# Kernel optimization log

Measured on AMD Instinct MI355X. Metric: run time of the kernel, lower is better.

## Reference

```python
import jax, jax.numpy as jnp
import numpy as np

B, N, C, H = 8, 1024, 768, 12
HD = C // H  # 64
SCALE = HD ** -0.5
T = 4
N_HALF = T // 2  # loop body with attention runs N_HALF times, V accumulates T times


def setup_inputs() -> dict:
    key = jax.random.key(0)
    ks = jax.random.split(key, 8)
    s = 0.02
    return {
        "x": jax.random.normal(ks[0], (B, N, C), jnp.float32),
        "Wqkv": jax.random.normal(ks[1], (3 * C, C), jnp.float32) * s,
        "Wfc1": jax.random.normal(ks[2], (HD, HD), jnp.float32) * s,
        "bfc1": jax.random.normal(ks[3], (HD,), jnp.float32) * s,
        "Wfc2": jax.random.normal(ks[4], (HD, HD), jnp.float32) * s,
        "bfc2": jax.random.normal(ks[5], (HD,), jnp.float32) * s,
        "Wproj": jax.random.normal(ks[6], (C, C), jnp.float32) * s,
        "bproj": jax.random.normal(ks[7], (C,), jnp.float32) * s,
    }


def reference(x, Wqkv, Wfc1, bfc1, Wfc2, bfc2, Wproj, bproj):
    b, n, c = x.shape
    # qkv projection (no bias), split into per-head q,k,v: [B,H,N,hd]
    qkv = (x @ Wqkv.T).reshape(b, n, 3, H, HD).transpose(2, 0, 3, 1, 4)
    q, k, v = qkv[0], qkv[1], qkv[2]
    # Loop body is stateless per timestep: first N_HALF steps each add the same
    # att_spk; all T steps add the same relu(v). Compute once, scale by counts.
    Q_spk = jax.nn.relu(q) @ Wfc1.T + bfc1  # [B,H,N,hd]
    K_spk = jax.nn.relu(k) @ Wfc2.T + bfc2  # [B,H,N,hd]
    att_spk = jax.nn.relu(jnp.einsum("bhqd,bhkd->bhqk", Q_spk, K_spk) * SCALE)
    att_rec = att_spk * float(N_HALF)   # accumulated over t < T/2
    V_rec = jax.nn.relu(v) * float(T)   # accumulated over all T steps
    att = jax.nn.softmax(att_rec, axis=-1)
    out = jnp.einsum("bhqk,bhkd->bhqd", att, V_rec)  # [B,H,N,hd]
    out = out.transpose(0, 2, 1, 3).reshape(b, n, c)
    return out @ Wproj.T + bproj
```

## Files before the change

### kernel.cpp

```cpp
#include <hip/hip_runtime.h>
#include <hip/hip_bf16.h>
#include <stdint.h>
#include <math.h>

#define BB   8
#define NN_  1024
#define CC   768
#define HH   12
#define HDD  64

typedef __attribute__((ext_vector_type(8))) short bf16x8;
typedef __attribute__((ext_vector_type(4))) float f32x4;
typedef __attribute__((ext_vector_type(16))) float f32x16;
typedef __attribute__((ext_vector_type(4))) float f32x4v;
typedef __attribute__((ext_vector_type(4))) unsigned short u16x4;

union FragU { unsigned int u[4]; bf16x8 b; };

__device__ __forceinline__ unsigned short f2bf(float f) {
    union { float f; unsigned int u; } v; v.f = f;
    unsigned int r = v.u + 0x7fffu + ((v.u >> 16) & 1u);
    return (unsigned short)(r >> 16);
}

#define CVTPK(d_, a_, b_) asm("v_cvt_pk_bf16_f32 %0, %1, %2" : "=v"(d_) : "v"(a_), "v"(b_))
#define SWAP32(a_, b_) asm("v_permlane32_swap_b32 %0, %1" : "+v"(a_), "+v"(b_))

#define GLDS(g_, l_) __builtin_amdgcn_global_load_lds( \
    (const __attribute__((address_space(1))) void*)(g_), \
    (__attribute__((address_space(3))) void*)(l_), 16, 0, 0)

#define MKFRAGS(P_, F0_, F1_) do {                                             \
    unsigned int c0,c1,c2,c3,c4,c5,c6,c7;                                      \
    CVTPK(c0, P_[0],  P_[1]);  CVTPK(c1, P_[2],  P_[3]);                       \
    CVTPK(c2, P_[4],  P_[5]);  CVTPK(c3, P_[6],  P_[7]);                       \
    CVTPK(c4, P_[8],  P_[9]);  CVTPK(c5, P_[10], P_[11]);                      \
    CVTPK(c6, P_[12], P_[13]); CVTPK(c7, P_[14], P_[15]);                      \
    SWAP32(c0, c2); SWAP32(c1, c3); SWAP32(c4, c6); SWAP32(c5, c7);            \
    FragU fu0_, fu1_;                                                          \
    fu0_.u[0]=c0; fu0_.u[1]=c1; fu0_.u[2]=c2; fu0_.u[3]=c3;                    \
    fu1_.u[0]=c4; fu1_.u[1]=c5; fu1_.u[2]=c6; fu1_.u[3]=c7;                    \
    F0_ = fu0_.b; F1_ = fu1_.b;                                                \
} while (0)

#define CVT_N0 1572864
#define CVT_N1 2015232
#define CVT_N2 2162688
#define CVT_N3 2163712
#define CVT_N4 2164736
__global__ void cvt_all(const float* __restrict__ x, const float* __restrict__ wqkv,
                        const float* __restrict__ wproj, const float* __restrict__ wf1,
                        const float* __restrict__ wf2,
                        unsigned short* __restrict__ xb, unsigned short* __restrict__ wqkvb,
                        unsigned short* __restrict__ wprojb, unsigned short* __restrict__ wf1b,
                        unsigned short* __restrict__ wf2b) {
    int i = blockIdx.x * blockDim.x + threadIdx.x;
    int stride = gridDim.x * blockDim.x;
    for (; i < CVT_N4; i += stride) {
        const f32x4v* src; u16x4* dst; int off;
        if (i < CVT_N0)      { src = (const f32x4v*)x;     dst = (u16x4*)xb;     off = i; }
        else if (i < CVT_N1) { src = (const f32x4v*)wqkv;  dst = (u16x4*)wqkvb;  off = i - CVT_N0; }
        else if (i < CVT_N2) { src = (const f32x4v*)wproj; dst = (u16x4*)wprojb; off = i - CVT_N1; }
        else if (i < CVT_N3) { src = (const f32x4v*)wf1;   dst = (u16x4*)wf1b;   off = i - CVT_N2; }
        else                 { src = (const f32x4v*)wf2;   dst = (u16x4*)wf2b;   off = i - CVT_N3; }
        f32x4v v = src[off];
        u16x4 o;
        o.x = f2bf(v.x); o.y = f2bf(v.y); o.z = f2bf(v.z); o.w = f2bf(v.w);
        dst[off] = o;
    }
}

__global__ __launch_bounds__(512, 1)
void qkv_spk_gemm(const unsigned short* __restrict__ X,
                  const unsigned short* __restrict__ Wqkv,
                  const unsigned short* __restrict__ Wf1,
                  const unsigned short* __restrict__ Wf2,
                  const float* __restrict__ bf1,
                  const float* __restrict__ bf2,
                  unsigned short* __restrict__ Rq,
                  unsigned short* __restrict__ Rk,
                  unsigned short* __restrict__ VT) {
    __shared__ short sA[3][256 * 64];
    __shared__ short sB[3][128 * 64];

    const int t    = threadIdx.x;
    const int wid  = t >> 6;
    const int lane = t & 63;
    const int l31  = lane & 31;
    const int hi5  = lane >> 5;
    const int fw   = wid >> 1;
    const int wn   = wid & 1;

    const int bid  = (int)blockIdx.x;
    const int lbid = (bid & 7) * 72 + (bid >> 3);
    const int bx   = lbid & 63;
    const int by   = lbid >> 6;
    const int F0   = by * 256;
    const int T0   = bx * 128;

#define STG(bi_, kt_) do {                                                     \
    const int k0_ = (kt_) * 64;                                                \
    _Pragma("unroll")                                                          \
    for (int i = 0; i < 4; i++) {                                              \
        int li_ = i * 512 + t;                                                 \
        int row_ = li_ >> 3, sl_ = li_ & 7;                                    \
        GLDS(Wqkv + (size_t)(F0 + row_) * 768 + k0_ + ((sl_ ^ (row_ & 7)) * 8),\
             &sA[bi_][li_ * 8]);                                               \
    }                                                                          \
    _Pragma("unroll")                                                          \
    for (int i = 0; i < 2; i++) {                                              \
        int li_ = i * 512 + t;                                                 \
        int row_ = li_ >> 3, sl_ = li_ & 7;                                    \
        GLDS(X + (size_t)(T0 + row_) * 768 + k0_ + ((sl_ ^ (row_ & 7)) * 8),   \
             &sB[bi_][li_ * 8]);                                               \
    }                                                                          \
} while (0)

    f32x16 acc[2][2];
#pragma unroll
    for (int fb = 0; fb < 2; fb++)
#pragma unroll
        for (int tb = 0; tb < 2; tb++)
#pragma unroll
            for (int r = 0; r < 16; r++) acc[fb][tb][r] = 0.f;

#define TILE(bc_, kt_) do {                                                    \
    if ((kt_) + 2 < 12) STG(((bc_) + 2) % 3, (kt_) + 2);                       \
    const char* ab_ = (const char*)sA[bc_];                                    \
    const char* bb_ = (const char*)sB[bc_];                                    \
    bf16x8 wf_[2][4], xf_[2][4];                                               \
    _Pragma("unroll")                                                          \
    for (int fb = 0; fb < 2; fb++) {                                           \
        int r_ = fw * 64 + fb * 32 + l31;                                      \
        _Pragma("unroll")                                                      \
        for (int ks = 0; ks < 4; ks++)                                         \
            wf_[fb][ks] = *(const bf16x8*)(ab_ + r_ * 128 +                    \
                (((ks * 2 + hi5) ^ (r_ & 7)) << 4));                           \
    }                                                                          \
    _Pragma("unroll")                                                          \
    for (int tb = 0; tb < 2; tb++) {                                           \
        int r_ = wn * 64 + tb * 32 + l31;                                      \
        _Pragma("unroll")                                                      \
        for (int ks = 0; ks < 4; ks++)                                         \
            xf_[tb][ks] = *(const bf16x8*)(bb_ + r_ * 128 +                    \
                (((ks * 2 + hi5) ^ (r_ & 7)) << 4));                           \
    }                                                                          \
    __builtin_amdgcn_s_setprio(1);                                             \
    _Pragma("unroll")                                                          \
    for (int ks = 0; ks < 4; ks++)                                             \
        _Pragma("unroll")                                                      \
        for (int fb = 0; fb < 2; fb++)                                         \
            _Pragma("unroll")                                                  \
            for (int tb = 0; tb < 2; tb++)                                     \
                acc[fb][tb] = __builtin_amdgcn_mfma_f32_32x32x16_bf16(         \
                    wf_[fb][ks], xf_[tb][ks], acc[fb][tb], 0, 0, 0);           \
    __builtin_amdgcn_s_setprio(0);                                             \
    asm volatile("s_waitcnt vmcnt(6)" ::: "memory");                           \
    __builtin_amdgcn_s_barrier();                                              \
} while (0)

    STG(0, 0);
    STG(1, 1);
    asm volatile("s_waitcnt vmcnt(6)" ::: "memory");
    __builtin_amdgcn_s_barrier();

#pragma unroll 1
    for (int kt3 = 0; kt3 < 12; kt3 += 3) {
        TILE(0, kt3);
        TILE(1, kt3 + 1);
        TILE(2, kt3 + 2);
    }
#undef TILE
#undef STG

    const int fbase = F0 + fw * 64;
    const int p  = fbase / 768;
    const int hh = (fbase - p * 768) >> 6;
    const int tok0 = T0 + wn * 64;
    const int b  = tok0 >> 10;
    const int n0 = tok0 & 1023;
    const int crow0 = 4 * hi5;

    if (p == 2) {
        const size_t vtb = ((size_t)(b * HH + hh)) * HDD * NN_;
#pragma unroll
        for (int fb = 0; fb < 2; fb++)
#pragma unroll
            for (int tb = 0; tb < 2; tb++)
#pragma unroll
                for (int r = 0; r < 16; r++) {
                    int d = fb * 32 + (r & 3) + 8 * (r >> 2) + crow0;
                    int n = n0 + tb * 32 + l31;
                    VT[vtb + (size_t)d * NN_ + n] = f2bf(4.f * fmaxf(acc[fb][tb][r], 0.f));
                }
    } else {
        const unsigned short* Wf = p ? Wf2 : Wf1;
        const float* bfp = p ? bf2 : bf1;
        unsigned short* R = p ? Rk : Rq;
        bf16x8 wfr[2][4];
#pragma unroll
        for (int dh = 0; dh < 2; dh++)
#pragma unroll
            for (int ks = 0; ks < 4; ks++)
                wfr[dh][ks] = *(const bf16x8*)&Wf[(size_t)(dh * 32 + l31) * HDD + ks * 16 + hi5 * 8];
        float bv0 = bfp[l31], bv1 = bfp[32 + l31];
        const size_t qkb = ((size_t)(b * HH + hh)) * NN_ * HDD;
#pragma unroll
        for (int tb = 0; tb < 2; tb++) {
            float pv0[16], pv1[16];
#pragma unroll
            for (int r = 0; r < 16; r++) {
                pv0[r] = fmaxf(acc[0][tb][r], 0.f);
                pv1[r] = fmaxf(acc[1][tb][r], 0.f);
            }
            bf16x8 pa0, pa1, pa2, pa3;
            MKFRAGS(pv0, pa0, pa1);
            MKFRAGS(pv1, pa2, pa3);
            f32x16 D0, D1;
#pragma unroll
            for (int r = 0; r < 16; r++) { D0[r] = 0.f; D1[r] = 0.f; }
            D0 = __builtin_amdgcn_mfma_f32_32x32x16_bf16(pa0, wfr[0][0], D0, 0, 0, 0);
            D0 = __builtin_amdgcn_mfma_f32_32x32x16_bf16(pa1, wfr[0][1], D0, 0, 0, 0);
            D0 = __builtin_amdgcn_mfma_f32_32x32x16_bf16(pa2, wfr[0][2], D0, 0, 0, 0);
            D0 = __builtin_amdgcn_mfma_f32_32x32x16_bf16(pa3, wfr[0][3], D0, 0, 0, 0);
            D1 = __builtin_amdgcn_mfma_f32_32x32x16_bf16(pa0, wfr[1][0], D1, 0, 0, 0);
            D1 = __builtin_amdgcn_mfma_f32_32x32x16_bf16(pa1, wfr[1][1], D1, 0, 0, 0);
            D1 = __builtin_amdgcn_mfma_f32_32x32x16_bf16(pa2, wfr[1][2], D1, 0, 0, 0);
            D1 = __builtin_amdgcn_mfma_f32_32x32x16_bf16(pa3, wfr[1][3], D1, 0, 0, 0);
#pragma unroll
            for (int r = 0; r < 16; r++) {
                int n = n0 + tb * 32 + (r & 3) + 8 * (r >> 2) + crow0;
                size_t rowb = qkb + (size_t)n * HDD;
                R[rowb + l31]      = f2bf(D0[r] + bv0);
                R[rowb + 32 + l31] = f2bf(D1[r] + bv1);
            }
        }
    }
}

__global__ __launch_bounds__(256, 2)
void attn_kernel(const unsigned short* __restrict__ Q,
                 const unsigned short* __restrict__ Kx,
                 const unsigned short* __restrict__ VT,
                 unsigned short* __restrict__ AO) {
    __shared__ short sK[2][64 * 64];
    __shared__ short sV[2][64 * 64];
    __shared__ float sinv[4][32];

    const int t    = threadIdx.x;
    const int lane = t & 63;
    const int wid  = t >> 6;
    const int l31  = lane & 31;
    const int hi5  = lane >> 5;

    const int bid = (int)blockIdx.x;
    const int lbid = (bid & 7) * 96 + (bid >> 3);
    const int bh = lbid >> 3;
    const int qt = lbid & 7;
    const int b = bh / HH, h = bh - b * HH;

    const unsigned short* Qs = Q  + (size_t)bh * NN_ * HDD;
    const unsigned short* Ks = Kx + (size_t)bh * NN_ * HDD;
    const unsigned short* Vt = VT + (size_t)bh * HDD * NN_;
    const int q0 = qt * 128 + wid * 32;

    bf16x8 qf[4];
#pragma unroll
    for (int ds = 0; ds < 4; ds++)
        qf[ds] = *(const bf16x8*)&Qs[(size_t)(q0 + l31) * HDD + ds * 16 + hi5 * 8];

    f32x16 O0, O1;
#pragma unroll
    for (int r = 0; r < 16; r++) { O0[r] = 0.f; O1[r] = 0.f; }
    float sumacc = 0.f;

    const int srow = t >> 3;
    const int sslot = t & 7;
    const int dstoff = ((t & 192)) * 8;

#define STAGE(buf_, kt_) do {                                                  \
    _Pragma("unroll")                                                          \
    for (int i = 0; i < 2; i++) {                                              \
        int row_ = srow + i * 32;                                              \
        int sl_  = (sslot ^ (row_ & 7)) << 3;                                  \
        const unsigned short* gk_ = Ks + (size_t)((kt_) * 64 + row_) * HDD + sl_; \
        const unsigned short* gv_ = Vt + (size_t)row_ * NN_ + (kt_) * 64 + sl_;   \
        GLDS(gk_, &sK[buf_][i * 2048 + dstoff]);                               \
        GLDS(gv_, &sV[buf_][i * 2048 + dstoff]);                               \
    }                                                                          \
} while (0)

    STAGE(0, 0);
    __syncthreads();

    int buf = 0;
    for (int kt = 0; kt < 16; ++kt) {
        if (kt < 15) STAGE(buf ^ 1, kt + 1);

        const char* kbase = (const char*)&sK[buf][0];
        const char* vbase = (const char*)&sV[buf][0];

        bf16x8 vbf[4][2];
#pragma unroll
        for (int ks = 0; ks < 4; ks++)
#pragma unroll
            for (int dt = 0; dt < 2; dt++) {
                int d = dt * 32 + l31;
                vbf[ks][dt] = *(const bf16x8*)(vbase + d * 128 +
                               ((ks * 32 + hi5 * 16) ^ ((d & 7) << 4)));
            }
        bf16x8 ka[2][4];
#pragma unroll
        for (int kt2 = 0; kt2 < 2; kt2++)
#pragma unroll
            for (int ds = 0; ds < 4; ds++) {
                int kk = kt2 * 32 + l31;
                ka[kt2][ds] = *(const bf16x8*)(kbase + kk * 128 +
                               ((ds * 32 + hi5 * 16) ^ ((kk & 7) << 4)));
            }

        f32x16 S0, S1;
#pragma unroll
        for (int r = 0; r < 16; r++) { S0[r] = 0.f; S1[r] = 0.f; }
#pragma unroll
        for (int ds = 0; ds < 4; ds++) {
            S0 = __builtin_amdgcn_mfma_f32_32x32x16_bf16(ka[0][ds], qf[ds], S0, 0, 0, 0);
            S1 = __builtin_amdgcn_mfma_f32_32x32x16_bf16(ka[1][ds], qf[ds], S1, 0, 0, 0);
        }

        float p0[16], p1[16];
#pragma unroll
        for (int r = 0; r < 16; r++) {
            p0[r] = exp2f(0.36067376f * fmaxf(S0[r], 0.f));
            p1[r] = exp2f(0.36067376f * fmaxf(S1[r], 0.f));
        }
        float s0 = 0.f, s1 = 0.f;
#pragma unroll
        for (int r = 0; r < 16; r++) { s0 += p0[r]; s1 += p1[r]; }
        sumacc += s0 + s1;

        bf16x8 paf0, paf1, paf2, paf3;
        MKFRAGS(p0, paf0, paf1);
        MKFRAGS(p1, paf2, paf3);

        O0 = __builtin_amdgcn_mfma_f32_32x32x16_bf16(paf0, vbf[0][0], O0, 0, 0, 0);
        O1 = __builtin_amdgcn_mfma_f32_32x32x16_bf16(paf0, vbf[0][1], O1, 0, 0, 0);
        O0 = __builtin_amdgcn_mfma_f32_32x32x16_bf16(paf1, vbf[1][0], O0, 0, 0, 0);
        O1 = __builtin_amdgcn_mfma_f32_32x32x16_bf16(paf1, vbf[1][1], O1, 0, 0, 0);
        O0 = __builtin_amdgcn_mfma_f32_32x32x16_bf16(paf2, vbf[2][0], O0, 0, 0, 0);
        O1 = __builtin_amdgcn_mfma_f32_32x32x16_bf16(paf2, vbf[2][1], O1, 0, 0, 0);
        O0 = __builtin_amdgcn_mfma_f32_32x32x16_bf16(paf3, vbf[3][0], O0, 0, 0, 0);
        O1 = __builtin_amdgcn_mfma_f32_32x32x16_bf16(paf3, vbf[3][1], O1, 0, 0, 0);

        __syncthreads();
        buf ^= 1;
    }
#undef STAGE

    float stot = sumacc + __shfl_xor(sumacc, 32, 64);
    float inv = 1.f / stot;
    if (l31 == lane) sinv[wid][l31] = inv;
    __syncthreads();

#pragma unroll
    for (int r = 0; r < 16; r++) {
        int qloc = (r & 3) + 8 * (r >> 2) + 4 * hi5;
        float iv = sinv[wid][qloc];
        size_t row = (size_t)(b * NN_ + q0 + qloc) * CC + h * HDD;
        AO[row + l31]      = f2bf(O0[r] * iv);
        AO[row + 32 + l31] = f2bf(O1[r] * iv);
    }
}

__global__ __launch_bounds__(256)
void proj_gemm(const unsigned short* __restrict__ A,
               const unsigned short* __restrict__ Bt,
               const float* __restrict__ bias,
               float* __restrict__ Out) {
    __shared__ short sA[128 * 32];
    __shared__ short sB[128 * 32];
    const int K = 768;
    const int lane = threadIdx.x & 63;
    const int wid  = threadIdx.x >> 6;
    const int wr = wid >> 1, wc = wid & 1;
    const int brow = blockIdx.x * 128;
    const int bcol = blockIdx.y * 128;
    const int t = threadIdx.x;

    f32x4 acc[4][4];
#pragma unroll
    for (int m = 0; m < 4; m++)
#pragma unroll
        for (int n = 0; n < 4; n++) acc[m][n] = (f32x4){0.f, 0.f, 0.f, 0.f};

    for (int k0 = 0; k0 < K; k0 += 32) {
#pragma unroll
        for (int i = 0; i < 2; i++) {
            int tt  = i * 256 + t;
            int row = tt >> 2;
            int kc  = (tt & 3) * 8;
            const unsigned short* ga = A  + (size_t)(brow + row) * K + k0 + kc;
            const unsigned short* gb = Bt + (size_t)(bcol + row) * K + k0 + kc;
            GLDS(ga, &sA[(i * 256 + wid * 64) * 8]);
            GLDS(gb, &sB[(i * 256 + wid * 64) * 8]);
        }
        __syncthreads();
        bf16x8 af[4], bfg[4];
#pragma unroll
        for (int m = 0; m < 4; m++) {
            int r = wr * 64 + m * 16 + (lane & 15);
            af[m] = *(const bf16x8*)&sA[r * 32 + (lane >> 4) * 8];
        }
#pragma unroll
        for (int n = 0; n < 4; n++) {
            int c = wc * 64 + n * 16 + (lane & 15);
            bfg[n] = *(const bf16x8*)&sB[c * 32 + (lane >> 4) * 8];
        }
#pragma unroll
        for (int m = 0; m < 4; m++)
#pragma unroll
            for (int n = 0; n < 4; n++)
                acc[m][n] = __builtin_amdgcn_mfma_f32_16x16x32_bf16(af[m], bfg[n], acc[m][n], 0, 0, 0);
        __syncthreads();
    }
#pragma unroll
    for (int m = 0; m < 4; m++)
#pragma unroll
        for (int n = 0; n < 4; n++) {
            int col = bcol + wc * 64 + n * 16 + (lane & 15);
            float bv = bias[col];
#pragma unroll
            for (int r = 0; r < 4; r++) {
                int row = brow + wr * 64 + m * 16 + (lane >> 4) * 4 + r;
                Out[(size_t)row * 768 + col] = acc[m][n][r] + bv;
            }
        }
}

extern "C" void kernel_launch(void* const* d_in, const int* in_sizes, int n_in,
                              void* d_out, int out_size, void* d_ws, size_t ws_size,
                              hipStream_t stream) {
    const float* x     = (const float*)d_in[0];
    const float* Wqkv  = (const float*)d_in[1];
    const float* Wfc1  = (const float*)d_in[2];
    const float* bfc1  = (const float*)d_in[3];
    const float* Wfc2  = (const float*)d_in[4];
    const float* bfc2  = (const float*)d_in[5];
    const float* Wproj = (const float*)d_in[6];
    const float* bproj = (const float*)d_in[7];
    float* out = (float*)d_out;

    char* ws = (char*)d_ws;
    const size_t SZ_XN = (size_t)8192 * 768 * 2;
    unsigned short* x_bf    = (unsigned short*)ws; ws += SZ_XN;
    unsigned short* wqkv_bf = (unsigned short*)ws; ws += (size_t)2304 * 768 * 2;
    unsigned short* wproj_bf= (unsigned short*)ws; ws += (size_t)768 * 768 * 2;
    unsigned short* wfc1_bf = (unsigned short*)ws; ws += 64 * 64 * 2;
    unsigned short* wfc2_bf = (unsigned short*)ws; ws += 64 * 64 * 2;
    unsigned short* Rq      = (unsigned short*)ws; ws += SZ_XN;
    unsigned short* Rk      = (unsigned short*)ws; ws += SZ_XN;
    unsigned short* VT      = (unsigned short*)ws; ws += SZ_XN;

    cvt_all<<<2048, 256, 0, stream>>>(x, Wqkv, Wproj, Wfc1, Wfc2,
                                      x_bf, wqkv_bf, wproj_bf, wfc1_bf, wfc2_bf);
    qkv_spk_gemm<<<576, 512, 0, stream>>>(x_bf, wqkv_bf, wfc1_bf, wfc2_bf,
                                          bfc1, bfc2, Rq, Rk, VT);
    attn_kernel<<<768, 256, 0, stream>>>(Rq, Rk, VT, x_bf);
    proj_gemm<<<dim3(64, 6), 256, 0, stream>>>(x_bf, wproj_bf, bproj, out);
}
```

Before: 138.7 us.

## Halve QKV GEMM k-tile to 32 so two blocks fit per CU

Shrinks the QKV GEMM's K step from 64 to 32. The LDS ring buffers are halved (two rows of 32 packed per 128-byte swizzled line) so that two 512-thread blocks can reside per CU, and launch bounds are raised to allow this. The pipeline now runs 24 phases with fewer loads in flight per stage, which adds twice as many barriers and halves the MFMA work between syncs in exchange for higher occupancy.

Result: no change. 137.6 us (-0.8%).

```diff
diff --git a/kernel.cpp b/kernel.cpp
--- a/kernel.cpp
+++ b/kernel.cpp
@@ -70,7 +70,7 @@
     }
 }
 
-__global__ __launch_bounds__(512, 1)
+__global__ __launch_bounds__(512, 2)
 void qkv_spk_gemm(const unsigned short* __restrict__ X,
                   const unsigned short* __restrict__ Wqkv,
                   const unsigned short* __restrict__ Wf1,
@@ -80,8 +80,8 @@
                   unsigned short* __restrict__ Rq,
                   unsigned short* __restrict__ Rk,
                   unsigned short* __restrict__ VT) {
-    __shared__ short sA[3][256 * 64];
-    __shared__ short sB[3][128 * 64];
+    __shared__ short sA[3][8192];
+    __shared__ short sB[3][4096];
 
     const int t    = threadIdx.x;
     const int wid  = t >> 6;
@@ -99,20 +99,19 @@
     const int T0   = bx * 128;
 
 #define STG(bi_, kt_) do {                                                     \
-    const int k0_ = (kt_) * 64;                                                \
-    _Pragma("unroll")                                                          \
-    for (int i = 0; i < 4; i++) {                                              \
-        int li_ = i * 512 + t;                                                 \
-        int row_ = li_ >> 3, sl_ = li_ & 7;                                    \
-        GLDS(Wqkv + (size_t)(F0 + row_) * 768 + k0_ + ((sl_ ^ (row_ & 7)) * 8),\
-             &sA[bi_][li_ * 8]);                                               \
-    }                                                                          \
     _Pragma("unroll")                                                          \
     for (int i = 0; i < 2; i++) {                                              \
         int li_ = i * 512 + t;                                                 \
-        int row_ = li_ >> 3, sl_ = li_ & 7;                                    \
-        GLDS(X + (size_t)(T0 + row_) * 768 + k0_ + ((sl_ ^ (row_ & 7)) * 8),   \
-             &sB[bi_][li_ * 8]);                                               \
+        int dr_ = li_ >> 3;                                                    \
+        int u_  = (li_ & 7) ^ (dr_ & 7);                                       \
+        GLDS(Wqkv + (size_t)(F0 + dr_ * 2 + (u_ >> 2)) * 768 + (kt_) * 32 + (u_ & 3) * 8, \
+             &sA[bi_][li_ * 8]);                                               \
+    }                                                                          \
+    {                                                                          \
+        int dr_ = t >> 3;                                                      \
+        int u_  = (t & 7) ^ (dr_ & 7);                                         \
+        GLDS(X + (size_t)(T0 + dr_ * 2 + (u_ >> 2)) * 768 + (kt_) * 32 + (u_ & 3) * 8, \
+             &sB[bi_][t * 8]);                                                 \
     }                                                                          \
 } while (0)
 
@@ -124,30 +123,32 @@
 #pragma unroll
             for (int r = 0; r < 16; r++) acc[fb][tb][r] = 0.f;
 
-#define TILE(bc_, kt_) do {                                                    \
-    if ((kt_) + 2 < 12) STG(((bc_) + 2) % 3, (kt_) + 2);                       \
+#define PH(bc_, kt_) do {                                                      \
+    if ((kt_) + 2 < 24) STG(((bc_) + 2) % 3, (kt_) + 2);                       \
     const char* ab_ = (const char*)sA[bc_];                                    \
     const char* bb_ = (const char*)sB[bc_];                                    \
-    bf16x8 wf_[2][4], xf_[2][4];                                               \
+    bf16x8 wf_[2][2], xf_[2][2];                                               \
     _Pragma("unroll")                                                          \
     for (int fb = 0; fb < 2; fb++) {                                           \
         int r_ = fw * 64 + fb * 32 + l31;                                      \
+        int dr_ = r_ >> 1;                                                     \
         _Pragma("unroll")                                                      \
-        for (int ks = 0; ks < 4; ks++)                                         \
-            wf_[fb][ks] = *(const bf16x8*)(ab_ + r_ * 128 +                    \
-                (((ks * 2 + hi5) ^ (r_ & 7)) << 4));                           \
+        for (int ks = 0; ks < 2; ks++)                                         \
+            wf_[fb][ks] = *(const bf16x8*)(ab_ + dr_ * 128 +                   \
+                ((((r_ & 1) * 4 + ks * 2 + hi5) ^ (dr_ & 7)) << 4));           \
     }                                                                          \
     _Pragma("unroll")                                                          \
     for (int tb = 0; tb < 2; tb++) {                                           \
         int r_ = wn * 64 + tb * 32 + l31;                                      \
+        int dr_ = r_ >> 1;                                                     \
         _Pragma("unroll")                                                      \
-        for (int ks = 0; ks < 4; ks++)                                         \
-            xf_[tb][ks] = *(const bf16x8*)(bb_ + r_ * 128 +                    \
-                (((ks * 2 + hi5) ^ (r_ & 7)) << 4));                           \
+        for (int ks = 0; ks < 2; ks++)                                         \
+            xf_[tb][ks] = *(const bf16x8*)(bb_ + dr_ * 128 +                   \
+                ((((r_ & 1) * 4 + ks * 2 + hi5) ^ (dr_ & 7)) << 4));           \
     }                                                                          \
     __builtin_amdgcn_s_setprio(1);                                             \
     _Pragma("unroll")                                                          \
-    for (int ks = 0; ks < 4; ks++)                                             \
+    for (int ks = 0; ks < 2; ks++)                                             \
         _Pragma("unroll")                                                      \
         for (int fb = 0; fb < 2; fb++)                                         \
             _Pragma("unroll")                                                  \
@@ -155,22 +156,22 @@
                 acc[fb][tb] = __builtin_amdgcn_mfma_f32_32x32x16_bf16(         \
                     wf_[fb][ks], xf_[tb][ks], acc[fb][tb], 0, 0, 0);           \
     __builtin_amdgcn_s_setprio(0);                                             \
-    asm volatile("s_waitcnt vmcnt(6)" ::: "memory");                           \
+    asm volatile("s_waitcnt vmcnt(3)" ::: "memory");                           \
     __builtin_amdgcn_s_barrier();                                              \
 } while (0)
 
     STG(0, 0);
     STG(1, 1);
-    asm volatile("s_waitcnt vmcnt(6)" ::: "memory");
+    asm volatile("s_waitcnt vmcnt(3)" ::: "memory");
     __builtin_amdgcn_s_barrier();
 
 #pragma unroll 1
-    for (int kt3 = 0; kt3 < 12; kt3 += 3) {
-        TILE(0, kt3);
-        TILE(1, kt3 + 1);
-        TILE(2, kt3 + 2);
-    }
-#undef TILE
+    for (int kt3 = 0; kt3 < 24; kt3 += 3) {
+        PH(0, kt3);
+        PH(1, kt3 + 1);
+        PH(2, kt3 + 2);
+    }
+#undef PH
 #undef STG
 
     const int fbase = F0 + fw * 64;
```
